# Kernel tuning notes

Measured on AMD Instinct MI355X. Metric: run time of the kernel, lower is better.

The kernel has to match this reference:

```python
import jax, jax.numpy as jnp
import numpy as np

B, N, H, F_IN, F_OUT = 16, 512, 8, 128, 128
NEG_SLOPE = 0.2


def setup_inputs() -> dict:
    key = jax.random.key(0)
    k_h, k_adj, k_bias, k_W, k_a = jax.random.split(key, 5)
    h = jax.random.normal(k_h, (B, N, F_IN), dtype=jnp.float32)
    # Binary adjacency (shared across batch); force self-loops so every row
    # of the masked softmax has at least one valid entry (avoids NaN rows).
    adj = jax.random.randint(k_adj, (N, N), 0, 2, dtype=jnp.int32)
    adj = adj.at[jnp.arange(N), jnp.arange(N)].set(1)
    bias_matrix = jax.random.normal(k_bias, (1, 1, N, N), dtype=jnp.float32)
    # Xavier-uniform-like init for params
    lim_W = float(np.sqrt(6.0 / (F_IN + F_OUT)))
    W = jax.random.uniform(k_W, (H, F_IN, F_OUT), minval=-lim_W, maxval=lim_W, dtype=jnp.float32)
    lim_a = float(np.sqrt(6.0 / (2 * F_OUT + 1)))
    a = jax.random.uniform(k_a, (H, 2 * F_OUT, 1), minval=-lim_a, maxval=lim_a, dtype=jnp.float32)
    return {"h": h, "adj": adj, "bias_matrix": bias_matrix, "W": W, "a": a}


def reference(h, adj, bias_matrix, W, a):
    # h: [B,N,Fin], adj: [N,N] int, bias_matrix: [1,1,N,N], W: [H,Fin,F], a: [H,2F,1]
    f = W.shape[-1]
    h_prime = jnp.einsum('bni,hio->bnho', h, W)  # [B,N,H,F]
    # e[b,i,j,h] = leakyrelu(a_h . concat(h_prime[b,i,h], h_prime[b,j,h]))
    # Decompose a into src/dst halves: identical math, avoids O(B*N*N*H*2F) cat.
    a_src = a[:, :f, 0]  # [H,F]
    a_dst = a[:, f:, 0]  # [H,F]
    s_src = jnp.einsum('bnhf,hf->bnh', h_prime, a_src)  # score contribution of node i
    s_dst = jnp.einsum('bnhf,hf->bnh', h_prime, a_dst)  # score contribution of node j
    e = jax.nn.leaky_relu(s_src[:, :, None, :] + s_dst[:, None, :, :], NEG_SLOPE)  # [B,N,N,H]
    e = e + bias_matrix[0, 0][None, :, :, None]  # bias broadcast over batch & heads
    mask = (adj != 0)[None, :, :, None]  # [1,N,N,1] -> broadcast [B,N,N,H]
    e = jnp.where(mask, e, -jnp.inf)
    attention = jax.nn.softmax(e, axis=2)  # softmax over neighbors j
    h_out = jnp.einsum('bijh,bjhf->bihf', attention, h_prime)  # [B,N,H,F]
    # concat=False -> mean over heads
    return h_out.mean(axis=2)  # [B,N,F]
```

## Files before the change

kernel.cpp:

```cpp
#include <hip/hip_runtime.h>
#include <hip/hip_bf16.h>

#define NB 16
#define NN 512
#define NH 8
#define NF 128
#define NEG_SLOPE 0.2f

typedef short bf16x8 __attribute__((ext_vector_type(8)));
typedef unsigned short u16x8 __attribute__((ext_vector_type(8)));
typedef float f32x4 __attribute__((ext_vector_type(4)));

__device__ inline unsigned short f2bf(float x) {
    unsigned int u = __float_as_uint(x);
    unsigned int r = (u + 0x7fffu + ((u >> 16) & 1u)) >> 16;
    return (unsigned short)r;
}
__device__ inline float bf2f(unsigned short u) {
    return __uint_as_float(((unsigned int)u) << 16);
}

__global__ __launch_bounds__(256) void prep_kernel(
    const int* __restrict__ adj, const float* __restrict__ bias,
    const float* __restrict__ W, const float* __restrict__ a,
    float* __restrict__ mb, float* __restrict__ wasrc, float* __restrict__ wadst)
{
    int t = blockIdx.x * 256 + threadIdx.x;
    if (t < NN * NN) mb[t] = (adj[t] != 0) ? bias[t] : -1.0e30f;
    if (t < NH * NF) {
        int hh = t >> 7, i = t & 127;
        const float* wrow = W + (hh * NF + i) * NF;
        const float* asr = a + hh * 2 * NF;
        const float* ads = asr + NF;
        float s1 = 0.f, s2 = 0.f;
        #pragma unroll 4
        for (int f = 0; f < NF; ++f) {
            float w = wrow[f];
            s1 = fmaf(w, asr[f], s1);
            s2 = fmaf(w, ads[f], s2);
        }
        wasrc[t] = s1; wadst[t] = s2;
    }
}

__global__ __launch_bounds__(256) void split_kernel(
    const float* __restrict__ h, const float* __restrict__ W,
    unsigned short* __restrict__ hHi, unsigned short* __restrict__ hLo,
    unsigned short* __restrict__ wtHi, unsigned short* __restrict__ wtLo)
{
    int t = blockIdx.x * 256 + threadIdx.x;
    if (t < NB * NN * NF) {
        float v = h[t];
        unsigned short hi = f2bf(v);
        hHi[t] = hi;
        hLo[t] = f2bf(v - bf2f(hi));
    } else {
        int u = t - NB * NN * NF;
        if (u < NH * NF * NF) {
            int fg = u >> 7, k = u & 127;
            float v = W[(size_t)(fg >> 7) * NF * NF + k * NF + (fg & 127)];
            unsigned short hi = f2bf(v);
            wtHi[u] = hi;
            wtLo[u] = f2bf(v - bf2f(hi));
        }
    }
}

__global__ __launch_bounds__(256) void score_kernel(
    const float* __restrict__ h, const float* __restrict__ wasrc,
    const float* __restrict__ wadst, float* __restrict__ ssrc, float* __restrict__ sdstT)
{
    __shared__ float wsm[2][NH * (NF + 4)];
    int tid = threadIdx.x;
    for (int u = tid; u < NH * NF; u += 256) {
        int hh = u >> 7, f = u & 127;
        wsm[0][hh * (NF + 4) + f] = wasrc[u];
        wsm[1][hh * (NF + 4) + f] = wadst[u];
    }
    __syncthreads();
    int t = blockIdx.x * 256 + tid;
    int hh = t & 7;
    int bn = t >> 3;
    int b = bn >> 9, n = bn & 511;
    const float4* hrow = (const float4*)(h + (size_t)bn * NF);
    const float4* w1 = (const float4*)(&wsm[0][hh * (NF + 4)]);
    const float4* w2 = (const float4*)(&wsm[1][hh * (NF + 4)]);
    float s1 = 0.f, s2 = 0.f;
    #pragma unroll
    for (int u = 0; u < NF / 4; ++u) {
        float4 hv = hrow[u], a1 = w1[u], a2 = w2[u];
        s1 += hv.x * a1.x + hv.y * a1.y + hv.z * a1.z + hv.w * a1.w;
        s2 += hv.x * a2.x + hv.y * a2.y + hv.z * a2.z + hv.w * a2.w;
    }
    ssrc[t] = s1;
    sdstT[((size_t)(b * NH + hh)) * NN + n] = s2;
}

__global__ __launch_bounds__(256) void hprime_kernel(
    const unsigned short* __restrict__ hHi, const unsigned short* __restrict__ hLo,
    const unsigned short* __restrict__ wtHi, const unsigned short* __restrict__ wtLo,
    unsigned short* __restrict__ hpT)
{
    int tid = threadIdx.x;
    int wave = tid >> 6, lane = tid & 63;
    int col = lane & 15, kg = lane >> 4;
    int f0 = blockIdx.y * 64 + wave * 16;
    int n0 = blockIdx.x * 64;

    const unsigned short* Ah = wtHi + (size_t)(f0 + col) * NF + kg * 8;
    const unsigned short* Al = wtLo + (size_t)(f0 + col) * NF + kg * 8;
    const unsigned short* Bh0 = hHi + (size_t)(n0 +  0 + col) * NF + kg * 8;
    const unsigned short* Bh1 = hHi + (size_t)(n0 + 16 + col) * NF + kg * 8;
    const unsigned short* Bh2 = hHi + (size_t)(n0 + 32 + col) * NF + kg * 8;
    const unsigned short* Bh3 = hHi + (size_t)(n0 + 48 + col) * NF + kg * 8;
    const unsigned short* Bl0 = hLo + (size_t)(n0 +  0 + col) * NF + kg * 8;
    const unsigned short* Bl1 = hLo + (size_t)(n0 + 16 + col) * NF + kg * 8;
    const unsigned short* Bl2 = hLo + (size_t)(n0 + 32 + col) * NF + kg * 8;
    const unsigned short* Bl3 = hLo + (size_t)(n0 + 48 + col) * NF + kg * 8;

    f32x4 acc0 = {0.f,0.f,0.f,0.f}, acc1 = {0.f,0.f,0.f,0.f};
    f32x4 acc2 = {0.f,0.f,0.f,0.f}, acc3 = {0.f,0.f,0.f,0.f};

    #pragma unroll
    for (int ks = 0; ks < 4; ++ks) {
        int off = ks * 32;
        bf16x8 ahi = *(const bf16x8*)(Ah + off);
        bf16x8 alo = *(const bf16x8*)(Al + off);
        bf16x8 b0h = *(const bf16x8*)(Bh0 + off);
        bf16x8 b1h = *(const bf16x8*)(Bh1 + off);
        bf16x8 b2h = *(const bf16x8*)(Bh2 + off);
        bf16x8 b3h = *(const bf16x8*)(Bh3 + off);
        bf16x8 b0l = *(const bf16x8*)(Bl0 + off);
        bf16x8 b1l = *(const bf16x8*)(Bl1 + off);
        bf16x8 b2l = *(const bf16x8*)(Bl2 + off);
        bf16x8 b3l = *(const bf16x8*)(Bl3 + off);
        acc0 = __builtin_amdgcn_mfma_f32_16x16x32_bf16(ahi, b0h, acc0, 0, 0, 0);
        acc1 = __builtin_amdgcn_mfma_f32_16x16x32_bf16(ahi, b1h, acc1, 0, 0, 0);
        acc2 = __builtin_amdgcn_mfma_f32_16x16x32_bf16(ahi, b2h, acc2, 0, 0, 0);
        acc3 = __builtin_amdgcn_mfma_f32_16x16x32_bf16(ahi, b3h, acc3, 0, 0, 0);
        acc0 = __builtin_amdgcn_mfma_f32_16x16x32_bf16(alo, b0h, acc0, 0, 0, 0);
        acc1 = __builtin_amdgcn_mfma_f32_16x16x32_bf16(alo, b1h, acc1, 0, 0, 0);
        acc2 = __builtin_amdgcn_mfma_f32_16x16x32_bf16(alo, b2h, acc2, 0, 0, 0);
        acc3 = __builtin_amdgcn_mfma_f32_16x16x32_bf16(alo, b3h, acc3, 0, 0, 0);
        acc0 = __builtin_amdgcn_mfma_f32_16x16x32_bf16(ahi, b0l, acc0, 0, 0, 0);
        acc1 = __builtin_amdgcn_mfma_f32_16x16x32_bf16(ahi, b1l, acc1, 0, 0, 0);
        acc2 = __builtin_amdgcn_mfma_f32_16x16x32_bf16(ahi, b2l, acc2, 0, 0, 0);
        acc3 = __builtin_amdgcn_mfma_f32_16x16x32_bf16(ahi, b3l, acc3, 0, 0, 0);
    }

    int b = n0 >> 9;
    int nin = n0 & 511;
    #pragma unroll
    for (int r = 0; r < 4; ++r) {
        int fg = f0 + kg * 4 + r;
        size_t base = ((size_t)b * (NH * NF) + fg) * NN + nin + col;
        hpT[base +  0] = f2bf(acc0[r]);
        hpT[base + 16] = f2bf(acc1[r]);
        hpT[base + 32] = f2bf(acc2[r]);
        hpT[base + 48] = f2bf(acc3[r]);
    }
}

__global__ __launch_bounds__(512, 8) void attn_kernel(
    const unsigned short* __restrict__ hpT, const float* __restrict__ mb,
    const float* __restrict__ ssrc, const float* __restrict__ sdstT,
    float* __restrict__ part)
{
    __shared__ unsigned short P[16][520];

    int bx = blockIdx.x;
    int half = bx & 1;
    int it = (bx >> 1) & 31;
    int b = bx >> 6;
    int i0 = it * 16;
    int tid = threadIdx.x;
    int lane = tid & 63, wave = tid >> 6;
    int col = lane & 15, kg = lane >> 4;

    f32x4 acc0 = {0.f,0.f,0.f,0.f}, acc1 = {0.f,0.f,0.f,0.f};

    for (int hq = 0; hq < 4; ++hq) {
        int head = half * 4 + hq;
        const float* sd = sdstT + (size_t)(b * NH + head) * NN;
        #pragma unroll
        for (int rr = 0; rr < 2; ++rr) {
            int i = wave * 2 + rr;
            int row = i0 + i;
            float s_i = ssrc[((size_t)(b * NN + row)) * NH + head];
            const float4* sd4 = (const float4*)(sd + lane * 8);
            const float4* mb4 = (const float4*)(mb + (size_t)row * NN + lane * 8);
            float4 sv0 = sd4[0], sv1 = sd4[1];
            float4 mv0 = mb4[0], mv1 = mb4[1];
            float p8[8];
            {
                float x;
                x = s_i + sv0.x; x = x > 0.f ? x : NEG_SLOPE * x; p8[0] = x + mv0.x;
                x = s_i + sv0.y; x = x > 0.f ? x : NEG_SLOPE * x; p8[1] = x + mv0.y;
                x = s_i + sv0.z; x = x > 0.f ? x : NEG_SLOPE * x; p8[2] = x + mv0.z;
                x = s_i + sv0.w; x = x > 0.f ? x : NEG_SLOPE * x; p8[3] = x + mv0.w;
                x = s_i + sv1.x; x = x > 0.f ? x : NEG_SLOPE * x; p8[4] = x + mv1.x;
                x = s_i + sv1.y; x = x > 0.f ? x : NEG_SLOPE * x; p8[5] = x + mv1.y;
                x = s_i + sv1.z; x = x > 0.f ? x : NEG_SLOPE * x; p8[6] = x + mv1.z;
                x = s_i + sv1.w; x = x > 0.f ? x : NEG_SLOPE * x; p8[7] = x + mv1.w;
            }
            float mx = fmaxf(fmaxf(fmaxf(p8[0], p8[1]), fmaxf(p8[2], p8[3])),
                             fmaxf(fmaxf(p8[4], p8[5]), fmaxf(p8[6], p8[7])));
            #pragma unroll
            for (int off = 32; off; off >>= 1) mx = fmaxf(mx, __shfl_xor(mx, off));
            float sum = 0.f;
            #pragma unroll
            for (int v = 0; v < 8; ++v) { p8[v] = __expf(p8[v] - mx); sum += p8[v]; }
            #pragma unroll
            for (int off = 32; off; off >>= 1) sum += __shfl_xor(sum, off);
            float rinv = 1.0f / sum;
            u16x8 pw;
            #pragma unroll
            for (int v = 0; v < 8; ++v) pw[v] = f2bf(p8[v] * rinv);
            *(u16x8*)&P[i][lane * 8] = pw;
        }
        __syncthreads();

        const unsigned short* Bp = hpT
            + ((size_t)(b * NH + head) * NF + wave * 16 + col) * NN + kg * 8;
        const unsigned short* Ap = &P[col][kg * 8];
        bf16x8 B0v = *(const bf16x8*)(Bp);
        bf16x8 B1v = *(const bf16x8*)(Bp + 32);
        #pragma unroll
        for (int ks = 0; ks < 8; ++ks) {
            bf16x8 a0 = *(const bf16x8*)(Ap + ks * 64);
            bf16x8 a1 = *(const bf16x8*)(Ap + ks * 64 + 32);
            bf16x8 nb0, nb1;
            if (ks < 7) {
                nb0 = *(const bf16x8*)(Bp + ks * 64 + 64);
                nb1 = *(const bf16x8*)(Bp + ks * 64 + 96);
            }
            acc0 = __builtin_amdgcn_mfma_f32_16x16x32_bf16(a0, B0v, acc0, 0, 0, 0);
            acc1 = __builtin_amdgcn_mfma_f32_16x16x32_bf16(a1, B1v, acc1, 0, 0, 0);
            if (ks < 7) { B0v = nb0; B1v = nb1; }
        }
        __syncthreads();
    }

    float* po = part + (size_t)half * (NB * NN * NF);
    #pragma unroll
    for (int r = 0; r < 4; ++r) {
        po[((size_t)(b * NN + i0 + kg * 4 + r)) * NF + wave * 16 + col] = acc0[r] + acc1[r];
    }
}

__global__ __launch_bounds__(256) void combine_kernel(
    const float* __restrict__ part, float* __restrict__ out)
{
    int t = blockIdx.x * 256 + threadIdx.x;
    float4 a = ((const float4*)part)[t];
    float4 c = ((const float4*)(part + (size_t)NB * NN * NF))[t];
    float4 o;
    o.x = (a.x + c.x) * 0.125f;
    o.y = (a.y + c.y) * 0.125f;
    o.z = (a.z + c.z) * 0.125f;
    o.w = (a.w + c.w) * 0.125f;
    ((float4*)out)[t] = o;
}

extern "C" void kernel_launch(void* const* d_in, const int* in_sizes, int n_in,
                              void* d_out, int out_size, void* d_ws, size_t ws_size,
                              hipStream_t stream)
{
    const float* h    = (const float*)d_in[0];
    const int*   adj  = (const int*)d_in[1];
    const float* bias = (const float*)d_in[2];
    const float* W    = (const float*)d_in[3];
    const float* a    = (const float*)d_in[4];
    float* out = (float*)d_out;

    char* ws = (char*)d_ws;
    unsigned short* hpT  = (unsigned short*)ws;                 ws += (size_t)NB * NH * NF * NN * 2;
    float* mb    = (float*)ws;                                  ws += (size_t)NN * NN * 4;
    float* ssrc  = (float*)ws;                                  ws += (size_t)NB * NN * NH * 4;
    float* sdstT = (float*)ws;                                  ws += (size_t)NB * NN * NH * 4;
    float* wasrc = (float*)ws;                                  ws += NH * NF * 4;
    float* wadst = (float*)ws;                                  ws += NH * NF * 4;
    unsigned short* hHi  = (unsigned short*)ws;                 ws += (size_t)NB * NN * NF * 2;
    unsigned short* hLo  = (unsigned short*)ws;                 ws += (size_t)NB * NN * NF * 2;
    unsigned short* wtHi = (unsigned short*)ws;                 ws += (size_t)NH * NF * NF * 2;
    unsigned short* wtLo = (unsigned short*)ws;                 ws += (size_t)NH * NF * NF * 2;
    float* part  = (float*)ws;                                  ws += (size_t)2 * NB * NN * NF * 4;

    hipLaunchKernelGGL(prep_kernel, dim3((NN * NN) / 256), dim3(256), 0, stream,
                       adj, bias, W, a, mb, wasrc, wadst);
    hipLaunchKernelGGL(split_kernel, dim3((NB * NN * NF + NH * NF * NF) / 256), dim3(256), 0, stream,
                       h, W, hHi, hLo, wtHi, wtLo);
    hipLaunchKernelGGL(score_kernel, dim3((NB * NN * NH) / 256), dim3(256), 0, stream,
                       h, wasrc, wadst, ssrc, sdstT);
    hipLaunchKernelGGL(hprime_kernel, dim3((NB * NN) / 64, (NH * NF) / 64), dim3(256), 0, stream,
                       hHi, hLo, wtHi, wtLo, hpT);
    hipLaunchKernelGGL(attn_kernel, dim3(NB * 32 * 2), dim3(512), 0, stream,
                       hpT, mb, ssrc, sdstT, part);
    hipLaunchKernelGGL(combine_kernel, dim3((NB * NN * NF / 4) / 256), dim3(256), 0, stream,
                       part, out);
}
```

Measured before the change: 191.0 us.

## Merge prep kernels, defer softmax normalization to MFMA row sums, atomically combine halves

Fuses the prep and split kernels into one launch. The attention kernel drops the per-row max and sum reductions: it stores unnormalized exp values and computes the row sums with extra MFMAs against a vector of ones, then divides after the matmul. The two head-halves are combined with atomicAdd into a zeroed output, which removes the partial buffer and the combine kernel but adds a memset and atomics. The hprime kernel's operand roles are also swapped so it writes vectorized stores. Skipping the max subtraction risks exp overflow for large scores.

```diff
diff --git a/kernel.cpp b/kernel.cpp
--- a/kernel.cpp
+++ b/kernel.cpp
@@ -20,13 +20,30 @@
     return __uint_as_float(((unsigned int)u) << 16);
 }
 
-__global__ __launch_bounds__(256) void prep_kernel(
-    const int* __restrict__ adj, const float* __restrict__ bias,
-    const float* __restrict__ W, const float* __restrict__ a,
-    float* __restrict__ mb, float* __restrict__ wasrc, float* __restrict__ wadst)
+__global__ __launch_bounds__(256) void prep_all_kernel(
+    const float* __restrict__ h, const int* __restrict__ adj,
+    const float* __restrict__ bias, const float* __restrict__ W,
+    const float* __restrict__ a,
+    float* __restrict__ mb,
+    unsigned short* __restrict__ hHi, unsigned short* __restrict__ hLo,
+    unsigned short* __restrict__ wtHi, unsigned short* __restrict__ wtLo,
+    float* __restrict__ wasrc, float* __restrict__ wadst)
 {
     int t = blockIdx.x * 256 + threadIdx.x;
+    {
+        float v = h[t];
+        unsigned short hi = f2bf(v);
+        hHi[t] = hi;
+        hLo[t] = f2bf(v - bf2f(hi));
+    }
     if (t < NN * NN) mb[t] = (adj[t] != 0) ? bias[t] : -1.0e30f;
+    if (t < NH * NF * NF) {
+        int fg = t >> 7, k = t & 127;
+        float v = W[(size_t)(fg >> 7) * NF * NF + k * NF + (fg & 127)];
+        unsigned short hi = f2bf(v);
+        wtHi[t] = hi;
+        wtLo[t] = f2bf(v - bf2f(hi));
+    }
     if (t < NH * NF) {
         int hh = t >> 7, i = t & 127;
         const float* wrow = W + (hh * NF + i) * NF;
@@ -43,29 +60,6 @@
     }
 }
 
-__global__ __launch_bounds__(256) void split_kernel(
-    const float* __restrict__ h, const float* __restrict__ W,
-    unsigned short* __restrict__ hHi, unsigned short* __restrict__ hLo,
-    unsigned short* __restrict__ wtHi, unsigned short* __restrict__ wtLo)
-{
-    int t = blockIdx.x * 256 + threadIdx.x;
-    if (t < NB * NN * NF) {
-        float v = h[t];
-        unsigned short hi = f2bf(v);
-        hHi[t] = hi;
-        hLo[t] = f2bf(v - bf2f(hi));
-    } else {
-        int u = t - NB * NN * NF;
-        if (u < NH * NF * NF) {
-            int fg = u >> 7, k = u & 127;
-            float v = W[(size_t)(fg >> 7) * NF * NF + k * NF + (fg & 127)];
-            unsigned short hi = f2bf(v);
-            wtHi[u] = hi;
-            wtLo[u] = f2bf(v - bf2f(hi));
-        }
-    }
-}
-
 __global__ __launch_bounds__(256) void score_kernel(
     const float* __restrict__ h, const float* __restrict__ wasrc,
     const float* __restrict__ wadst, float* __restrict__ ssrc, float* __restrict__ sdstT)
@@ -96,7 +90,7 @@
     sdstT[((size_t)(b * NH + hh)) * NN + n] = s2;
 }
 
-__global__ __launch_bounds__(256) void hprime_kernel(
+__global__ __launch_bounds__(256, 4) void hprime_kernel(
     const unsigned short* __restrict__ hHi, const unsigned short* __restrict__ hLo,
     const unsigned short* __restrict__ wtHi, const unsigned short* __restrict__ wtLo,
     unsigned short* __restrict__ hpT)
@@ -104,67 +98,53 @@
     int tid = threadIdx.x;
     int wave = tid >> 6, lane = tid & 63;
     int col = lane & 15, kg = lane >> 4;
-    int f0 = blockIdx.y * 64 + wave * 16;
     int n0 = blockIdx.x * 64;
-
-    const unsigned short* Ah = wtHi + (size_t)(f0 + col) * NF + kg * 8;
-    const unsigned short* Al = wtLo + (size_t)(f0 + col) * NF + kg * 8;
-    const unsigned short* Bh0 = hHi + (size_t)(n0 +  0 + col) * NF + kg * 8;
-    const unsigned short* Bh1 = hHi + (size_t)(n0 + 16 + col) * NF + kg * 8;
-    const unsigned short* Bh2 = hHi + (size_t)(n0 + 32 + col) * NF + kg * 8;
-    const unsigned short* Bh3 = hHi + (size_t)(n0 + 48 + col) * NF + kg * 8;
-    const unsigned short* Bl0 = hLo + (size_t)(n0 +  0 + col) * NF + kg * 8;
-    const unsigned short* Bl1 = hLo + (size_t)(n0 + 16 + col) * NF + kg * 8;
-    const unsigned short* Bl2 = hLo + (size_t)(n0 + 32 + col) * NF + kg * 8;
-    const unsigned short* Bl3 = hLo + (size_t)(n0 + 48 + col) * NF + kg * 8;
-
-    f32x4 acc0 = {0.f,0.f,0.f,0.f}, acc1 = {0.f,0.f,0.f,0.f};
-    f32x4 acc2 = {0.f,0.f,0.f,0.f}, acc3 = {0.f,0.f,0.f,0.f};
-
-    #pragma unroll
+    int ftile = blockIdx.y * 4 + wave;
+    int fbase = ftile * 16;
+
+    const unsigned short* Bh = wtHi + (size_t)(fbase + col) * NF + kg * 8;
+    const unsigned short* Bl = wtLo + (size_t)(fbase + col) * NF + kg * 8;
+    const unsigned short* Ah = hHi + (size_t)(n0 + col) * NF + kg * 8;
+    const unsigned short* Al = hLo + (size_t)(n0 + col) * NF + kg * 8;
+
+    f32x4 acc[4];
+    #pragma unroll
+    for (int q = 0; q < 4; ++q) acc[q] = (f32x4){0.f, 0.f, 0.f, 0.f};
+
+    #pragma unroll 2
     for (int ks = 0; ks < 4; ++ks) {
         int off = ks * 32;
-        bf16x8 ahi = *(const bf16x8*)(Ah + off);
-        bf16x8 alo = *(const bf16x8*)(Al + off);
-        bf16x8 b0h = *(const bf16x8*)(Bh0 + off);
-        bf16x8 b1h = *(const bf16x8*)(Bh1 + off);
-        bf16x8 b2h = *(const bf16x8*)(Bh2 + off);
-        bf16x8 b3h = *(const bf16x8*)(Bh3 + off);
-        bf16x8 b0l = *(const bf16x8*)(Bl0 + off);
-        bf16x8 b1l = *(const bf16x8*)(Bl1 + off);
-        bf16x8 b2l = *(const bf16x8*)(Bl2 + off);
-        bf16x8 b3l = *(const bf16x8*)(Bl3 + off);
-        acc0 = __builtin_amdgcn_mfma_f32_16x16x32_bf16(ahi, b0h, acc0, 0, 0, 0);
-        acc1 = __builtin_amdgcn_mfma_f32_16x16x32_bf16(ahi, b1h, acc1, 0, 0, 0);
-        acc2 = __builtin_amdgcn_mfma_f32_16x16x32_bf16(ahi, b2h, acc2, 0, 0, 0);
-        acc3 = __builtin_amdgcn_mfma_f32_16x16x32_bf16(ahi, b3h, acc3, 0, 0, 0);
-        acc0 = __builtin_amdgcn_mfma_f32_16x16x32_bf16(alo, b0h, acc0, 0, 0, 0);
-        acc1 = __builtin_amdgcn_mfma_f32_16x16x32_bf16(alo, b1h, acc1, 0, 0, 0);
-        acc2 = __builtin_amdgcn_mfma_f32_16x16x32_bf16(alo, b2h, acc2, 0, 0, 0);
-        acc3 = __builtin_amdgcn_mfma_f32_16x16x32_bf16(alo, b3h, acc3, 0, 0, 0);
-        acc0 = __builtin_amdgcn_mfma_f32_16x16x32_bf16(ahi, b0l, acc0, 0, 0, 0);
-        acc1 = __builtin_amdgcn_mfma_f32_16x16x32_bf16(ahi, b1l, acc1, 0, 0, 0);
-        acc2 = __builtin_amdgcn_mfma_f32_16x16x32_bf16(ahi, b2l, acc2, 0, 0, 0);
-        acc3 = __builtin_amdgcn_mfma_f32_16x16x32_bf16(ahi, b3l, acc3, 0, 0, 0);
+        bf16x8 bh = *(const bf16x8*)(Bh + off);
+        bf16x8 bl = *(const bf16x8*)(Bl + off);
+        #pragma unroll
+        for (int q = 0; q < 4; ++q) {
+            bf16x8 ah = *(const bf16x8*)(Ah + (size_t)q * 16 * NF + off);
+            bf16x8 al = *(const bf16x8*)(Al + (size_t)q * 16 * NF + off);
+            acc[q] = __builtin_amdgcn_mfma_f32_16x16x32_bf16(ah, bh, acc[q], 0, 0, 0);
+            acc[q] = __builtin_amdgcn_mfma_f32_16x16x32_bf16(al, bh, acc[q], 0, 0, 0);
+            acc[q] = __builtin_amdgcn_mfma_f32_16x16x32_bf16(ah, bl, acc[q], 0, 0, 0);
+        }
     }
 
     int b = n0 >> 9;
-    int nin = n0 & 511;
-    #pragma unroll
-    for (int r = 0; r < 4; ++r) {
-        int fg = f0 + kg * 4 + r;
-        size_t base = ((size_t)b * (NH * NF) + fg) * NN + nin + col;
-        hpT[base +  0] = f2bf(acc0[r]);
-        hpT[base + 16] = f2bf(acc1[r]);
-        hpT[base + 32] = f2bf(acc2[r]);
-        hpT[base + 48] = f2bf(acc3[r]);
+    int fg = fbase + col;
+    size_t rowBase = ((size_t)b * (NH * NF) + fg) * NN;
+    #pragma unroll
+    for (int q = 0; q < 4; ++q) {
+        int n = (n0 & 511) + q * 16 + kg * 4;
+        ushort4 u;
+        u.x = f2bf(acc[q][0]);
+        u.y = f2bf(acc[q][1]);
+        u.z = f2bf(acc[q][2]);
+        u.w = f2bf(acc[q][3]);
+        *(ushort4*)&hpT[rowBase + n] = u;
     }
 }
 
 __global__ __launch_bounds__(512, 8) void attn_kernel(
     const unsigned short* __restrict__ hpT, const float* __restrict__ mb,
     const float* __restrict__ ssrc, const float* __restrict__ sdstT,
-    float* __restrict__ part)
+    float* __restrict__ out)
 {
     __shared__ unsigned short P[16][520];
 
@@ -177,7 +157,10 @@
     int lane = tid & 63, wave = tid >> 6;
     int col = lane & 15, kg = lane >> 4;
 
-    f32x4 acc0 = {0.f,0.f,0.f,0.f}, acc1 = {0.f,0.f,0.f,0.f};
+    const short one_bf = (short)0x3f80;
+    const bf16x8 vone = {one_bf, one_bf, one_bf, one_bf, one_bf, one_bf, one_bf, one_bf};
+
+    f32x4 accT = {0.f, 0.f, 0.f, 0.f};
 
     for (int hq = 0; hq < 4; ++hq) {
         int head = half * 4 + hq;
@@ -191,31 +174,19 @@
             const float4* mb4 = (const float4*)(mb + (size_t)row * NN + lane * 8);
             float4 sv0 = sd4[0], sv1 = sd4[1];
             float4 mv0 = mb4[0], mv1 = mb4[1];
-            float p8[8];
-            {
-                float x;
-                x = s_i + sv0.x; x = x > 0.f ? x : NEG_SLOPE * x; p8[0] = x + mv0.x;
-                x = s_i + sv0.y; x = x > 0.f ? x : NEG_SLOPE * x; p8[1] = x + mv0.y;
-                x = s_i + sv0.z; x = x > 0.f ? x : NEG_SLOPE * x; p8[2] = x + mv0.z;
-                x = s_i + sv0.w; x = x > 0.f ? x : NEG_SLOPE * x; p8[3] = x + mv0.w;
-                x = s_i + sv1.x; x = x > 0.f ? x : NEG_SLOPE * x; p8[4] = x + mv1.x;
-                x = s_i + sv1.y; x = x > 0.f ? x : NEG_SLOPE * x; p8[5] = x + mv1.y;
-                x = s_i + sv1.z; x = x > 0.f ? x : NEG_SLOPE * x; p8[6] = x + mv1.z;
-                x = s_i + sv1.w; x = x > 0.f ? x : NEG_SLOPE * x; p8[7] = x + mv1.w;
-            }
-            float mx = fmaxf(fmaxf(fmaxf(p8[0], p8[1]), fmaxf(p8[2], p8[3])),
-                             fmaxf(fmaxf(p8[4], p8[5]), fmaxf(p8[6], p8[7])));
-            #pragma unroll
-            for (int off = 32; off; off >>= 1) mx = fmaxf(mx, __shfl_xor(mx, off));
-            float sum = 0.f;
-            #pragma unroll
-            for (int v = 0; v < 8; ++v) { p8[v] = __expf(p8[v] - mx); sum += p8[v]; }
-            #pragma unroll
-            for (int off = 32; off; off >>= 1) sum += __shfl_xor(sum, off);
-            float rinv = 1.0f / sum;
+            float p[8];
+            float x;
+            x = s_i + sv0.x; x = x > 0.f ? x : NEG_SLOPE * x; p[0] = __expf(x + mv0.x);
+            x = s_i + sv0.y; x = x > 0.f ? x : NEG_SLOPE * x; p[1] = __expf(x + mv0.y);
+            x = s_i + sv0.z; x = x > 0.f ? x : NEG_SLOPE * x; p[2] = __expf(x + mv0.z);
+            x = s_i + sv0.w; x = x > 0.f ? x : NEG_SLOPE * x; p[3] = __expf(x + mv0.w);
+            x = s_i + sv1.x; x = x > 0.f ? x : NEG_SLOPE * x; p[4] = __expf(x + mv1.x);
+            x = s_i + sv1.y; x = x > 0.f ? x : NEG_SLOPE * x; p[5] = __expf(x + mv1.y);
+            x = s_i + sv1.z; x = x > 0.f ? x : NEG_SLOPE * x; p[6] = __expf(x + mv1.z);
+            x = s_i + sv1.w; x = x > 0.f ? x : NEG_SLOPE * x; p[7] = __expf(x + mv1.w);
             u16x8 pw;
             #pragma unroll
-            for (int v = 0; v < 8; ++v) pw[v] = f2bf(p8[v] * rinv);
+            for (int v = 0; v < 8; ++v) pw[v] = f2bf(p[v]);
             *(u16x8*)&P[i][lane * 8] = pw;
         }
         __syncthreads();
@@ -223,8 +194,11 @@
         const unsigned short* Bp = hpT
             + ((size_t)(b * NH + head) * NF + wave * 16 + col) * NN + kg * 8;
         const unsigned short* Ap = &P[col][kg * 8];
+        f32x4 acc0 = {0.f,0.f,0.f,0.f}, acc1 = {0.f,0.f,0.f,0.f};
+        f32x4 accS0 = {0.f,0.f,0.f,0.f}, accS1 = {0.f,0.f,0.f,0.f};
         bf16x8 B0v = *(const bf16x8*)(Bp);
         bf16x8 B1v = *(const bf16x8*)(Bp + 32);
+        __builtin_amdgcn_s_setprio(1);
         #pragma unroll
         for (int ks = 0; ks < 8; ++ks) {
             bf16x8 a0 = *(const bf16x8*)(Ap + ks * 64);
@@ -234,32 +208,24 @@
                 nb0 = *(const bf16x8*)(Bp + ks * 64 + 64);
                 nb1 = *(const bf16x8*)(Bp + ks * 64 + 96);
             }
-            acc0 = __builtin_amdgcn_mfma_f32_16x16x32_bf16(a0, B0v, acc0, 0, 0, 0);
-            acc1 = __builtin_amdgcn_mfma_f32_16x16x32_bf16(a1, B1v, acc1, 0, 0, 0);
+            acc0  = __builtin_amdgcn_mfma_f32_16x16x32_bf16(a0, B0v,  acc0,  0, 0, 0);
+            acc1  = __builtin_amdgcn_mfma_f32_16x16x32_bf16(a1, B1v,  acc1,  0, 0, 0);
+            accS0 = __builtin_amdgcn_mfma_f32_16x16x32_bf16(a0, vone, accS0, 0, 0, 0);
+            accS1 = __builtin_amdgcn_mfma_f32_16x16x32_bf16(a1, vone, accS1, 0, 0, 0);
             if (ks < 7) { B0v = nb0; B1v = nb1; }
         }
+        __builtin_amdgcn_s_setprio(0);
+        #pragma unroll
+        for (int r = 0; r < 4; ++r)
+            accT[r] += (acc0[r] + acc1[r]) / (accS0[r] + accS1[r]);
         __syncthreads();
     }
 
-    float* po = part + (size_t)half * (NB * NN * NF);
     #pragma unroll
     for (int r = 0; r < 4; ++r) {
-        po[((size_t)(b * NN + i0 + kg * 4 + r)) * NF + wave * 16 + col] = acc0[r] + acc1[r];
-    }
-}
-
-__global__ __launch_bounds__(256) void combine_kernel(
-    const float* __restrict__ part, float* __restrict__ out)
-{
-    int t = blockIdx.x * 256 + threadIdx.x;
-    float4 a = ((const float4*)part)[t];
-    float4 c = ((const float4*)(part + (size_t)NB * NN * NF))[t];
-    float4 o;
-    o.x = (a.x + c.x) * 0.125f;
-    o.y = (a.y + c.y) * 0.125f;
-    o.z = (a.z + c.z) * 0.125f;
-    o.w = (a.w + c.w) * 0.125f;
-    ((float4*)out)[t] = o;
+        atomicAdd(&out[((size_t)(b * NN + i0 + kg * 4 + r)) * NF + wave * 16 + col],
+                  accT[r] * 0.125f);
+    }
 }
 
 extern "C" void kernel_launch(void* const* d_in, const int* in_sizes, int n_in,
@@ -274,28 +240,24 @@
     float* out = (float*)d_out;
 
     char* ws = (char*)d_ws;
-    unsigned short* hpT  = (unsigned short*)ws;                 ws += (size_t)NB * NH * NF * NN * 2;
-    float* mb    = (float*)ws;                                  ws += (size_t)NN * NN * 4;
-    float* ssrc  = (float*)ws;                                  ws += (size_t)NB * NN * NH * 4;
-    float* sdstT = (float*)ws;                                  ws += (size_t)NB * NN * NH * 4;
-    float* wasrc = (float*)ws;                                  ws += NH * NF * 4;
-    float* wadst = (float*)ws;                                  ws += NH * NF * 4;
-    unsigned short* hHi  = (unsigned short*)ws;                 ws += (size_t)NB * NN * NF * 2;
-    unsigned short* hLo  = (unsigned short*)ws;                 ws += (size_t)NB * NN * NF * 2;
-    unsigned short* wtHi = (unsigned short*)ws;                 ws += (size_t)NH * NF * NF * 2;
-    unsigned short* wtLo = (unsigned short*)ws;                 ws += (size_t)NH * NF * NF * 2;
-    float* part  = (float*)ws;                                  ws += (size_t)2 * NB * NN * NF * 4;
-
-    hipLaunchKernelGGL(prep_kernel, dim3((NN * NN) / 256), dim3(256), 0, stream,
-                       adj, bias, W, a, mb, wasrc, wadst);
-    hipLaunchKernelGGL(split_kernel, dim3((NB * NN * NF + NH * NF * NF) / 256), dim3(256), 0, stream,
-                       h, W, hHi, hLo, wtHi, wtLo);
+    unsigned short* hpT  = (unsigned short*)ws;   ws += (size_t)NB * NH * NF * NN * 2;
+    float* mb    = (float*)ws;                    ws += (size_t)NN * NN * 4;
+    float* ssrc  = (float*)ws;                    ws += (size_t)NB * NN * NH * 4;
+    float* sdstT = (float*)ws;                    ws += (size_t)NB * NN * NH * 4;
+    float* wasrc = (float*)ws;                    ws += NH * NF * 4;
+    float* wadst = (float*)ws;                    ws += NH * NF * 4;
+    unsigned short* hHi  = (unsigned short*)ws;   ws += (size_t)NB * NN * NF * 2;
+    unsigned short* hLo  = (unsigned short*)ws;   ws += (size_t)NB * NN * NF * 2;
+    unsigned short* wtHi = (unsigned short*)ws;   ws += (size_t)NH * NF * NF * 2;
+    unsigned short* wtLo = (unsigned short*)ws;   ws += (size_t)NH * NF * NF * 2;
+
+    hipLaunchKernelGGL(prep_all_kernel, dim3((NB * NN * NF) / 256), dim3(256), 0, stream,
+                       h, adj, bias, W, a, mb, hHi, hLo, wtHi, wtLo, wasrc, wadst);
     hipLaunchKernelGGL(score_kernel, dim3((NB * NN * NH) / 256), dim3(256), 0, stream,
                        h, wasrc, wadst, ssrc, sdstT);
     hipLaunchKernelGGL(hprime_kernel, dim3((NB * NN) / 64, (NH * NF) / 64), dim3(256), 0, stream,
                        hHi, hLo, wtHi, wtLo, hpT);
+    hipMemsetAsync(d_out, 0, (size_t)out_size * sizeof(float), stream);
     hipLaunchKernelGGL(attn_kernel, dim3(NB * 32 * 2), dim3(512), 0, stream,
-                       hpT, mb, ssrc, sdstT, part);
-    hipLaunchKernelGGL(combine_kernel, dim3((NB * NN * NF / 4) / 256), dim3(256), 0, stream,
-                       part, out);
-}
+                       hpT, mb, ssrc, sdstT, out);
+}
```

After: 213.1 us. +11.6%, slower.
